# Kernel tuning notes

Hardware: AMD Instinct MI355X
Metric: run time of the kernel (lower is better)

## Reference

```python
import jax, jax.numpy as jnp
import numpy as np

B, L, D, O = 8, 512, 256, 64  # batch, seq_len, in_dim, out_dim


def setup_inputs() -> dict:
    key = jax.random.key(0)
    k1, k2, k3 = jax.random.split(key, 3)
    x1 = jax.random.normal(k1, (B, L, 1, D), dtype=jnp.float32)  # head states
    x2 = jax.random.normal(k2, (B, 1, L, D), dtype=jnp.float32)  # dependent states
    # U: (out_dim, in_dim+1, in_dim+1); torch init is orthogonal then zeros the
    # flattened last column -- we use scaled normal with the same zeroed entry.
    U = jax.random.normal(k3, (O, D + 1, D + 1), dtype=jnp.float32) / np.sqrt(D + 1)
    U = U.reshape(O, -1).at[:, -1].set(0.0).reshape(O, D + 1, D + 1)
    return {"x1": x1, "x2": x2, "U": U}


def reference(x1, x2, U):
    # Bias-augment: append constant 1 to the feature dim (torch: cat([x, const])).
    x1a = jnp.concatenate([x1, jnp.ones((*x1.shape[:-1], 1), x1.dtype)], axis=-1)[:, :, 0, :]  # (B,L,D+1)
    x2a = jnp.concatenate([x2, jnp.ones((*x2.shape[:-1], 1), x2.dtype)], axis=-1)[:, 0, :, :]  # (B,L,D+1)
    # Torch loop: first matmul contracts U's LAST axis (j) with x1, second
    # contracts the remaining axis (i) with x2.
    t = jnp.einsum('oij,blj->bloi', U, x1a)        # (B,L,O,D+1)
    out = jnp.einsum('bloi,bmi->blmo', t, x2a)     # (B,L,L,O)
    return out
```

## Files before the change

kernel.cpp:

```cpp
#include <hip/hip_runtime.h>
#include <stdint.h>

#define B_  8
#define L_  512
#define Dk  256
#define O_  64
#define DP  257
#define IP  264
#define N1  (O_ * IP)
#define M1  (B_ * L_)

typedef __attribute__((ext_vector_type(8))) short bf16x8;
typedef __attribute__((ext_vector_type(4))) float f32x4;

__device__ __forceinline__ unsigned short f2bf(float f) {
    union { float f; unsigned u; } v; v.f = f;
    return (unsigned short)((v.u + 0x7fffu + ((v.u >> 16) & 1u)) >> 16);
}
__device__ __forceinline__ float bf2f(unsigned short h) {
    union { unsigned u; float f; } v; v.u = ((unsigned)h) << 16;
    return v.f;
}
__device__ __forceinline__ void gload16(const void* g, void* l) {
    __builtin_amdgcn_global_load_lds(
        (const __attribute__((address_space(1))) unsigned int*)g,
        (__attribute__((address_space(3))) unsigned int*)l, 16, 0, 0);
}

__global__ void cvt_x(const float* __restrict__ x1, const float* __restrict__ x2,
                      unsigned short* __restrict__ x1b, unsigned short* __restrict__ x2b) {
    int idx = blockIdx.x * 256 + threadIdx.x;
    const int half = (M1 * Dk) / 4;
    const float4* src; unsigned short* dst; int g;
    if (idx < half) { src = (const float4*)x1; dst = x1b; g = idx; }
    else            { src = (const float4*)x2; dst = x2b; g = idx - half; }
    float4 v = src[g];
    ushort4 w; w.x = f2bf(v.x); w.y = f2bf(v.y); w.z = f2bf(v.z); w.w = f2bf(v.w);
    *(ushort4*)&dst[g * 4] = w;
}

__global__ void cvt_u(const float* __restrict__ U, unsigned short* __restrict__ W2,
                      float* __restrict__ Ubias) {
    int t = blockIdx.x * 256 + threadIdx.x;
    int r = t >> 6; int j4 = (t & 63) << 2;
    int o = r / IP, i = r % IP;
    ushort4 w;
    if (i < DP) {
        const float* up = U + ((size_t)o * DP + i) * DP + j4;
        w.x = f2bf(up[0]); w.y = f2bf(up[1]); w.z = f2bf(up[2]); w.w = f2bf(up[3]);
        if (j4 == 0) Ubias[r] = U[((size_t)o * DP + i) * DP + 256];
    } else {
        w.x = w.y = w.z = w.w = 0;
        if (j4 == 0) Ubias[r] = 0.f;
    }
    *(ushort4*)&W2[(size_t)r * Dk + j4] = w;
}

__launch_bounds__(256)
__global__ void gemm1(const unsigned short* __restrict__ A,
                      const unsigned short* __restrict__ Bw,
                      const float* __restrict__ bias,
                      unsigned short* __restrict__ C) {
    __shared__ __align__(16) unsigned short As[128 * 32];
    __shared__ __align__(16) unsigned short Bs[128 * 32];
    const int tid = threadIdx.x, wave = tid >> 6, lane = tid & 63;
    const int m0 = blockIdx.y * 128, n0 = blockIdx.x * 128;
    const int wm = (wave >> 1) * 64, wn = (wave & 1) * 64;
    const int lrow = lane & 15, lq = lane >> 4;

    f32x4 acc[4][4] = {};
    for (int k0 = 0; k0 < Dk; k0 += 32) {
#pragma unroll
        for (int p = 0; p < 2; ++p) {
            int c = p * 256 + wave * 64 + lane;
            gload16(A  + (size_t)(m0 + (c >> 2)) * Dk + k0 + ((c & 3) << 3),
                    &As[(p * 256 + wave * 64) * 8]);
            gload16(Bw + (size_t)(n0 + (c >> 2)) * Dk + k0 + ((c & 3) << 3),
                    &Bs[(p * 256 + wave * 64) * 8]);
        }
        __syncthreads();
        bf16x8 af[4], bfr[4];
#pragma unroll
        for (int mt = 0; mt < 4; ++mt)
            af[mt] = *(const bf16x8*)&As[(wm + mt * 16 + lrow) * 32 + lq * 8];
#pragma unroll
        for (int nt = 0; nt < 4; ++nt)
            bfr[nt] = *(const bf16x8*)&Bs[(wn + nt * 16 + lrow) * 32 + lq * 8];
#pragma unroll
        for (int mt = 0; mt < 4; ++mt)
#pragma unroll
            for (int nt = 0; nt < 4; ++nt)
                acc[mt][nt] = __builtin_amdgcn_mfma_f32_16x16x32_bf16(
                    af[mt], bfr[nt], acc[mt][nt], 0, 0, 0);
        __syncthreads();
    }
#pragma unroll
    for (int mt = 0; mt < 4; ++mt)
#pragma unroll
        for (int nt = 0; nt < 4; ++nt) {
            int n = n0 + wn + nt * 16 + lrow;
            float bv = bias[n];
#pragma unroll
            for (int r = 0; r < 4; ++r) {
                int m = m0 + wm + mt * 16 + lq * 4 + r;
                C[(size_t)m * N1 + n] = f2bf(acc[mt][nt][r] + bv);
            }
        }
}

__launch_bounds__(256)
__global__ void gemm2(const unsigned short* __restrict__ X2b,
                      const unsigned short* __restrict__ T,
                      float* __restrict__ out) {
    __shared__ __align__(16) unsigned short As[128 * 32];
    __shared__ __align__(16) unsigned short Bs[64 * 32];
    const int tid = threadIdx.x, wave = tid >> 6, lane = tid & 63;
    const int bl = blockIdx.y;
    const int b  = bl >> 9;
    const int m0 = blockIdx.x * 128;
    const unsigned short* Ap = X2b + (size_t)b * (L_ * Dk);
    const unsigned short* Tp = T + (size_t)bl * N1;
    const int wm = (wave >> 1) * 64, wn = (wave & 1) * 32;
    const int lrow = lane & 15, lq = lane >> 4;

    f32x4 acc[4][2] = {};
    for (int k0 = 0; k0 < Dk; k0 += 32) {
#pragma unroll
        for (int p = 0; p < 2; ++p) {
            int c = p * 256 + wave * 64 + lane;
            gload16(Ap + (size_t)(m0 + (c >> 2)) * Dk + k0 + ((c & 3) << 3),
                    &As[(p * 256 + wave * 64) * 8]);
        }
        {
            int c = wave * 64 + lane;
            gload16(Tp + (size_t)(c >> 2) * IP + k0 + ((c & 3) << 3),
                    &Bs[(wave * 64) * 8]);
        }
        __syncthreads();
        bf16x8 af[4], bfr[2];
#pragma unroll
        for (int mt = 0; mt < 4; ++mt)
            af[mt] = *(const bf16x8*)&As[(wm + mt * 16 + lrow) * 32 + lq * 8];
#pragma unroll
        for (int nt = 0; nt < 2; ++nt)
            bfr[nt] = *(const bf16x8*)&Bs[(wn + nt * 16 + lrow) * 32 + lq * 8];
#pragma unroll
        for (int mt = 0; mt < 4; ++mt)
#pragma unroll
            for (int nt = 0; nt < 2; ++nt)
                acc[mt][nt] = __builtin_amdgcn_mfma_f32_16x16x32_bf16(
                    af[mt], bfr[nt], acc[mt][nt], 0, 0, 0);
        __syncthreads();
    }
#pragma unroll
    for (int nt = 0; nt < 2; ++nt) {
        int o = wn + nt * 16 + lrow;
        float bv = bf2f(Tp[o * IP + 256]);
#pragma unroll
        for (int mt = 0; mt < 4; ++mt)
#pragma unroll
            for (int r = 0; r < 4; ++r) {
                int m = m0 + wm + mt * 16 + lq * 4 + r;
                out[((size_t)bl * 512 + m) * 64 + o] = acc[mt][nt][r] + bv;
            }
    }
}

extern "C" void kernel_launch(void* const* d_in, const int* in_sizes, int n_in,
                              void* d_out, int out_size, void* d_ws, size_t ws_size,
                              hipStream_t stream) {
    const float* x1 = (const float*)d_in[0];
    const float* x2 = (const float*)d_in[1];
    const float* U  = (const float*)d_in[2];
    float* out = (float*)d_out;

    char* ws = (char*)d_ws;
    unsigned short* x1b  = (unsigned short*)(ws);
    unsigned short* x2b  = (unsigned short*)(ws + 2097152);
    unsigned short* W2   = (unsigned short*)(ws + 4194304);
    float*          Ubias= (float*)        (ws + 4194304 + 8650752);
    unsigned short* T    = (unsigned short*)(ws + 4194304 + 8650752 + 67584);

    hipLaunchKernelGGL(cvt_x, dim3(2048), dim3(256), 0, stream, x1, x2, x1b, x2b);
    hipLaunchKernelGGL(cvt_u, dim3((N1 * 64) / 256), dim3(256), 0, stream, U, W2, Ubias);
    hipLaunchKernelGGL(gemm1, dim3(N1 / 128, M1 / 128), dim3(256), 0, stream, x1b, W2, Ubias, T);
    hipLaunchKernelGGL(gemm2, dim3(L_ / 128, M1), dim3(256), 0, stream, x2b, T, out);
}
```

Baseline: 812.9 us.

## Drop LDS staging, load MFMA fragments from global, remap blocks per XCD

```diff
diff --git a/kernel.cpp b/kernel.cpp
--- a/kernel.cpp
+++ b/kernel.cpp
@@ -20,11 +20,6 @@
 __device__ __forceinline__ float bf2f(unsigned short h) {
     union { unsigned u; float f; } v; v.u = ((unsigned)h) << 16;
     return v.f;
-}
-__device__ __forceinline__ void gload16(const void* g, void* l) {
-    __builtin_amdgcn_global_load_lds(
-        (const __attribute__((address_space(1))) unsigned int*)g,
-        (__attribute__((address_space(3))) unsigned int*)l, 16, 0, 0);
 }
 
 __global__ void cvt_x(const float* __restrict__ x1, const float* __restrict__ x2,
@@ -61,108 +56,94 @@
                       const unsigned short* __restrict__ Bw,
                       const float* __restrict__ bias,
                       unsigned short* __restrict__ C) {
-    __shared__ __align__(16) unsigned short As[128 * 32];
-    __shared__ __align__(16) unsigned short Bs[128 * 32];
+    const int f = blockIdx.x;
+    const int xcd = f & 7, idx = f >> 3;
+    const int m0 = (xcd * 4 + (idx & 3)) * 128;
+    const int n0 = (idx >> 2) * 128;
     const int tid = threadIdx.x, wave = tid >> 6, lane = tid & 63;
-    const int m0 = blockIdx.y * 128, n0 = blockIdx.x * 128;
     const int wm = (wave >> 1) * 64, wn = (wave & 1) * 64;
     const int lrow = lane & 15, lq = lane >> 4;
+    const unsigned short* Ab = A  + (size_t)(m0 + wm + lrow) * Dk + lq * 8;
+    const unsigned short* Bb = Bw + (size_t)(n0 + wn + lrow) * Dk + lq * 8;
 
     f32x4 acc[4][4] = {};
+#pragma unroll
     for (int k0 = 0; k0 < Dk; k0 += 32) {
-#pragma unroll
-        for (int p = 0; p < 2; ++p) {
-            int c = p * 256 + wave * 64 + lane;
-            gload16(A  + (size_t)(m0 + (c >> 2)) * Dk + k0 + ((c & 3) << 3),
-                    &As[(p * 256 + wave * 64) * 8]);
-            gload16(Bw + (size_t)(n0 + (c >> 2)) * Dk + k0 + ((c & 3) << 3),
-                    &Bs[(p * 256 + wave * 64) * 8]);
-        }
-        __syncthreads();
         bf16x8 af[4], bfr[4];
 #pragma unroll
         for (int mt = 0; mt < 4; ++mt)
-            af[mt] = *(const bf16x8*)&As[(wm + mt * 16 + lrow) * 32 + lq * 8];
+            af[mt] = *(const bf16x8*)(Ab + mt * (16 * Dk) + k0);
 #pragma unroll
         for (int nt = 0; nt < 4; ++nt)
-            bfr[nt] = *(const bf16x8*)&Bs[(wn + nt * 16 + lrow) * 32 + lq * 8];
+            bfr[nt] = *(const bf16x8*)(Bb + nt * (16 * Dk) + k0);
 #pragma unroll
         for (int mt = 0; mt < 4; ++mt)
 #pragma unroll
             for (int nt = 0; nt < 4; ++nt)
                 acc[mt][nt] = __builtin_amdgcn_mfma_f32_16x16x32_bf16(
                     af[mt], bfr[nt], acc[mt][nt], 0, 0, 0);
-        __syncthreads();
     }
 #pragma unroll
-    for (int mt = 0; mt < 4; ++mt)
+    for (int nt = 0; nt < 4; ++nt) {
+        const int n = n0 + wn + nt * 16 + lrow;
+        const float bv = bias[n];
 #pragma unroll
-        for (int nt = 0; nt < 4; ++nt) {
-            int n = n0 + wn + nt * 16 + lrow;
-            float bv = bias[n];
+        for (int mt = 0; mt < 4; ++mt) {
+            const int m = m0 + wm + mt * 16 + lq * 4;
 #pragma unroll
-            for (int r = 0; r < 4; ++r) {
-                int m = m0 + wm + mt * 16 + lq * 4 + r;
-                C[(size_t)m * N1 + n] = f2bf(acc[mt][nt][r] + bv);
-            }
+            for (int r = 0; r < 4; ++r)
+                C[(size_t)(m + r) * N1 + n] = f2bf(acc[mt][nt][r] + bv);
         }
+    }
 }
 
 __launch_bounds__(256)
 __global__ void gemm2(const unsigned short* __restrict__ X2b,
                       const unsigned short* __restrict__ T,
                       float* __restrict__ out) {
-    __shared__ __align__(16) unsigned short As[128 * 32];
-    __shared__ __align__(16) unsigned short Bs[64 * 32];
+    const int f = blockIdx.x;
+    const int xcd = f & 7, idx = f >> 3;
+    const int b  = xcd;
+    const int l  = idx >> 1;
+    const int bl = (b << 9) + l;
+    const int m0 = (idx & 1) << 8;
     const int tid = threadIdx.x, wave = tid >> 6, lane = tid & 63;
-    const int bl = blockIdx.y;
-    const int b  = bl >> 9;
-    const int m0 = blockIdx.x * 128;
-    const unsigned short* Ap = X2b + (size_t)b * (L_ * Dk);
+    const int wm = wave << 6;
+    const int lrow = lane & 15, lq = lane >> 4;
+    const unsigned short* Ap = X2b + (size_t)b * (L_ * Dk)
+                             + (size_t)(m0 + wm + lrow) * Dk + lq * 8;
     const unsigned short* Tp = T + (size_t)bl * N1;
-    const int wm = (wave >> 1) * 64, wn = (wave & 1) * 32;
-    const int lrow = lane & 15, lq = lane >> 4;
+    const unsigned short* Bp = Tp + (size_t)lrow * IP + lq * 8;
 
-    f32x4 acc[4][2] = {};
+    f32x4 acc[4][4] = {};
+#pragma unroll
     for (int k0 = 0; k0 < Dk; k0 += 32) {
-#pragma unroll
-        for (int p = 0; p < 2; ++p) {
-            int c = p * 256 + wave * 64 + lane;
-            gload16(Ap + (size_t)(m0 + (c >> 2)) * Dk + k0 + ((c & 3) << 3),
-                    &As[(p * 256 + wave * 64) * 8]);
-        }
-        {
-            int c = wave * 64 + lane;
-            gload16(Tp + (size_t)(c >> 2) * IP + k0 + ((c & 3) << 3),
-                    &Bs[(wave * 64) * 8]);
-        }
-        __syncthreads();
-        bf16x8 af[4], bfr[2];
+        bf16x8 af[4], bfr[4];
 #pragma unroll
         for (int mt = 0; mt < 4; ++mt)
-            af[mt] = *(const bf16x8*)&As[(wm + mt * 16 + lrow) * 32 + lq * 8];
+            af[mt] = *(const bf16x8*)(Ap + mt * (16 * Dk) + k0);
 #pragma unroll
-        for (int nt = 0; nt < 2; ++nt)
-            bfr[nt] = *(const bf16x8*)&Bs[(wn + nt * 16 + lrow) * 32 + lq * 8];
+        for (int nt = 0; nt < 4; ++nt)
+            bfr[nt] = *(const bf16x8*)(Bp + nt * (16 * IP) + k0);
 #pragma unroll
         for (int mt = 0; mt < 4; ++mt)
 #pragma unroll
-            for (int nt = 0; nt < 2; ++nt)
+            for (int nt = 0; nt < 4; ++nt)
                 acc[mt][nt] = __builtin_amdgcn_mfma_f32_16x16x32_bf16(
                     af[mt], bfr[nt], acc[mt][nt], 0, 0, 0);
-        __syncthreads();
     }
+    float* op = out + (size_t)bl * (512 * 64);
 #pragma unroll
-    for (int nt = 0; nt < 2; ++nt) {
-        int o = wn + nt * 16 + lrow;
-        float bv = bf2f(Tp[o * IP + 256]);
+    for (int nt = 0; nt < 4; ++nt) {
+        const int o = nt * 16 + lrow;
+        const float bv = bf2f(Tp[o * IP + 256]);
 #pragma unroll
-        for (int mt = 0; mt < 4; ++mt)
+        for (int mt = 0; mt < 4; ++mt) {
+            const int m = m0 + wm + mt * 16 + lq * 4;
 #pragma unroll
-            for (int r = 0; r < 4; ++r) {
-                int m = m0 + wm + mt * 16 + lq * 4 + r;
-                out[((size_t)bl * 512 + m) * 64 + o] = acc[mt][nt][r] + bv;
-            }
+            for (int r = 0; r < 4; ++r)
+                op[(size_t)(m + r) * 64 + o] = acc[mt][nt][r] + bv;
+        }
     }
 }
 
@@ -183,6 +164,6 @@
 
     hipLaunchKernelGGL(cvt_x, dim3(2048), dim3(256), 0, stream, x1, x2, x1b, x2b);
     hipLaunchKernelGGL(cvt_u, dim3((N1 * 64) / 256), dim3(256), 0, stream, U, W2, Ubias);
-    hipLaunchKernelGGL(gemm1, dim3(N1 / 128, M1 / 128), dim3(256), 0, stream, x1b, W2, Ubias, T);
-    hipLaunchKernelGGL(gemm2, dim3(L_ / 128, M1), dim3(256), 0, stream, x2b, T, out);
+    hipLaunchKernelGGL(gemm1, dim3(4224), dim3(256), 0, stream, x1b, W2, Ubias, T);
+    hipLaunchKernelGGL(gemm2, dim3(8192), dim3(256), 0, stream, x2b, T, out);
 }
```

Result: slower. 928.8 us (+14.3%).
